# Optimization experiments

Measured on AMD Instinct MI355X. Metric: run time of the kernel, lower is better.

Reference implementation:

```python
import jax, jax.numpy as jnp
import numpy as np

POOL = (7, 7)


def crop_and_resize(image, boxes, box_idx, crop_size):
    """Faithful jnp port of tf.image.crop_and_resize (bilinear, extrapolation_value=0).

    image: [B, H, W, C]; boxes: [N, 4] normalized (y1, x1, y2, x2); box_idx: [N] int.
    Returns [N, ph, pw, C].
    """
    H, W = image.shape[1], image.shape[2]
    ph, pw = crop_size
    y1, x1, y2, x2 = boxes[:, 0], boxes[:, 1], boxes[:, 2], boxes[:, 3]
    iy = jnp.arange(ph, dtype=image.dtype)
    ix = jnp.arange(pw, dtype=image.dtype)
    # sample coords in source-pixel space, TF convention for crop_size > 1
    ys = y1[:, None] * (H - 1) + iy[None, :] * ((y2 - y1)[:, None] * (H - 1) / (ph - 1))  # [N, ph]
    xs = x1[:, None] * (W - 1) + ix[None, :] * ((x2 - x1)[:, None] * (W - 1) / (pw - 1))  # [N, pw]
    vy = (ys >= 0) & (ys <= H - 1)
    vx = (xs >= 0) & (xs <= W - 1)
    y0 = jnp.floor(ys)
    x0 = jnp.floor(xs)
    wy = (ys - y0)[:, :, None, None]   # [N, ph, 1, 1]
    wx = (xs - x0)[:, None, :, None]   # [N, 1, pw, 1]
    y0i = jnp.clip(y0, 0, H - 1).astype(jnp.int32)
    y1i = jnp.clip(y0 + 1, 0, H - 1).astype(jnp.int32)  # when ys is integral, wy==0 so clamp is harmless
    x0i = jnp.clip(x0, 0, W - 1).astype(jnp.int32)
    x1i = jnp.clip(x0 + 1, 0, W - 1).astype(jnp.int32)
    b = box_idx[:, None, None]

    def g(yi, xi):
        return image[b, yi[:, :, None], xi[:, None, :], :]  # [N, ph, pw, C]

    top = g(y0i, x0i) * (1 - wx) + g(y0i, x1i) * wx
    bot = g(y1i, x0i) * (1 - wx) + g(y1i, x1i) * wx
    out = top * (1 - wy) + bot * wy
    valid = (vy[:, :, None] & vx[:, None, :])[..., None]
    return jnp.where(valid, out, jnp.zeros((), image.dtype))


def setup_inputs() -> dict:
    key = jax.random.key(0)
    kb, kp, k3, k4, k5 = jax.random.split(key, 5)
    B, N, C = 2, 1000, 256
    # valid normalized boxes: per-axis sorted uniforms -> y1 <= y2, x1 <= x2
    raw = jax.random.uniform(kb, (B, N, 2, 2), dtype=jnp.float32)  # [..., (y|x), (lo,hi)]
    raw = jnp.sort(raw, axis=-1)
    boxes = jnp.stack([raw[..., 0, 0], raw[..., 1, 0], raw[..., 0, 1], raw[..., 1, 1]], axis=-1)
    return {
        "boxes": boxes,
        "positive_indices": jax.random.randint(kp, (B, N), 0, 2, dtype=jnp.int32),
        "p3": jax.random.normal(k3, (B, 128, 128, C), dtype=jnp.float32),
        "p4": jax.random.normal(k4, (B, 64, 64, C), dtype=jnp.float32),
        "p5": jax.random.normal(k5, (B, 32, 32, C), dtype=jnp.float32),
        "config": 0,
    }


def reference(boxes, positive_indices, p3, p4, p5, config):
    B, N = boxes.shape[0], boxes.shape[1]
    ph, pw = POOL
    h = boxes[..., 2] - boxes[..., 0]
    w = boxes[..., 3] - boxes[..., 1]
    # roi_level = clip(ceil(5 + log2(h*w)), 3, 5); clip in float first (log2(0) -> -inf)
    lvl = jnp.ceil(5.0 + jnp.log(h * w) / jnp.log(2.0))
    roi_level = jnp.clip(lvl, 3.0, 5.0).astype(jnp.int32)  # [B, N]
    boxes_flat = jax.lax.stop_gradient(boxes.reshape(B * N, 4))  # boxes get no grad in original
    lvl_flat = roi_level.reshape(B * N)
    box_idx = jnp.repeat(jnp.arange(B, dtype=jnp.int32), N)
    C = p3.shape[-1]
    pooled = jnp.zeros((B * N, ph, pw, C), dtype=p3.dtype)
    for level, feat in zip((3, 4, 5), (p3, p4, p5)):
        crop = crop_and_resize(feat, boxes_flat, box_idx, POOL)
        mask = (lvl_flat == level)[:, None, None, None]
        pooled = jnp.where(mask, crop, pooled)
    return pooled.reshape(B, N, ph, pw, C)
```

## Files before the change

### kernel.cpp

```cpp
#include <hip/hip_runtime.h>
#include <math.h>


#define N_PER_B 1000
#define NBOX    2000
#define CCH     256
#define PH      7
#define PW      7

typedef float f4 __attribute__((ext_vector_type(4)));

__global__ __launch_bounds__(448, 2) void pyramid_roi_align_kernel(
    const float* __restrict__ boxes,
    const float* __restrict__ p3,
    const float* __restrict__ p4,
    const float* __restrict__ p5,
    float* __restrict__ out)
{
    const int box  = blockIdx.x;
    const int iy   = threadIdx.x >> 6;
    const int lane = threadIdx.x & 63;
    const int c    = lane * 4;

    const float y1 = boxes[box * 4 + 0];
    const float x1 = boxes[box * 4 + 1];
    const float y2 = boxes[box * 4 + 2];
    const float x2 = boxes[box * 4 + 3];
    const float h  = y2 - y1;
    const float w  = x2 - x1;

    const float lvl  = ceilf(5.0f + logf(h * w) / 0.69314718055994530942f);
    const float lvlc = fminf(fmaxf(lvl, 3.0f), 5.0f);
    const int level  = (int)lvlc;

    const float* feat;
    int H;
    if (level <= 3)      { feat = p3; H = 128; }
    else if (level == 4) { feat = p4; H = 64;  }
    else                 { feat = p5; H = 32;  }
    const int W = H;

    const int b = (box >= N_PER_B) ? 1 : 0;
    feat += (size_t)b * H * W * CCH;

    const float Hm1 = (float)(H - 1);
    const float Wm1 = (float)(W - 1);

    const float ys = y1 * Hm1 + (float)iy * (h * Hm1 / 6.0f);
    const bool  vy = (ys >= 0.0f) && (ys <= Hm1);

    const float y0f = floorf(ys);
    const float wy  = ys - y0f;
    const float omwy = 1.0f - wy;

    const int y0i = (int)fminf(fmaxf(y0f,        0.0f), Hm1);
    const int y1i = (int)fminf(fmaxf(y0f + 1.0f, 0.0f), Hm1);

    const float* row0 = feat + (size_t)y0i * W * CCH + c;
    const float* row1 = feat + (size_t)y1i * W * CCH + c;

    const float xstep = w * Wm1 / 6.0f;

    int   x0i[PW], x1i[PW];
    float wxv[PW];
    bool  vx[PW];
#pragma unroll
    for (int ix = 0; ix < PW; ++ix) {
        const float xs = x1 * Wm1 + (float)ix * xstep;
        vx[ix] = (xs >= 0.0f) && (xs <= Wm1);
        const float x0f = floorf(xs);
        wxv[ix] = xs - x0f;
        x0i[ix] = (int)fminf(fmaxf(x0f,        0.0f), Wm1);
        x1i[ix] = (int)fminf(fmaxf(x0f + 1.0f, 0.0f), Wm1);
    }

    f4 v00[PW], v01[PW], v10[PW], v11[PW];
#pragma unroll
    for (int ix = 0; ix < PW; ++ix) {
        v00[ix] = *(const f4*)(row0 + (size_t)x0i[ix] * CCH);
        v01[ix] = *(const f4*)(row0 + (size_t)x1i[ix] * CCH);
        v10[ix] = *(const f4*)(row1 + (size_t)x0i[ix] * CCH);
        v11[ix] = *(const f4*)(row1 + (size_t)x1i[ix] * CCH);
    }

    float* dst_base = out + ((size_t)box * (PH * PW) + (size_t)iy * PW) * CCH + c;

#pragma unroll
    for (int ix = 0; ix < PW; ++ix) {
        const float wx   = wxv[ix];
        const float omwx = 1.0f - wx;

        f4 res = (v00[ix] * omwx + v01[ix] * wx) * omwy
               + (v10[ix] * omwx + v11[ix] * wx) * wy;

        if (!(vy && vx[ix])) res = (f4)(0.0f);

        __builtin_nontemporal_store(res, (f4*)(dst_base + (size_t)ix * CCH));
    }
}

extern "C" void kernel_launch(void* const* d_in, const int* in_sizes, int n_in,
                              void* d_out, int out_size, void* d_ws, size_t ws_size,
                              hipStream_t stream) {
    const float* boxes = (const float*)d_in[0];
    const float* p3 = (const float*)d_in[2];
    const float* p4 = (const float*)d_in[3];
    const float* p5 = (const float*)d_in[4];
    float* out = (float*)d_out;

    hipLaunchKernelGGL(pyramid_roi_align_kernel, dim3(NBOX), dim3(448), 0, stream,
                       boxes, p3, p4, p5, out);
}
```

Measured before the change: 171.2 us.

## Bucket boxes by level, batch and y-band and swizzle blocks across XCDs

Adds a single-block pre-pass that bucket-sorts boxes by pyramid level, batch index and vertical center band into a permutation held in workspace. The main kernel reads boxes through this permutation, and a block-id swizzle gives each XCD a contiguous chunk of sorted boxes, so boxes that sample the same feature rows share an L2. The output store also changes from nontemporal to a normal store. In exchange it adds an extra kernel launch and a serial prefix sum, and it depends on workspace being available.

Result: slower. 177.2 us (+3.5%).

```diff
diff --git a/kernel.cpp b/kernel.cpp
--- a/kernel.cpp
+++ b/kernel.cpp
@@ -8,16 +8,75 @@
 #define PH      7
 #define PW      7
 
+#define NXCD    8
+#define CHUNK   (NBOX / NXCD)
+
+#define NBUCKET 96
+
 typedef float f4 __attribute__((ext_vector_type(4)));
+
+__device__ __forceinline__ int box_level(float h, float w) {
+    const float lvl  = ceilf(5.0f + logf(h * w) / 0.69314718055994530942f);
+    const float lvlc = fminf(fmaxf(lvl, 3.0f), 5.0f);
+    return (int)lvlc;
+}
+
+__global__ __launch_bounds__(1024) void sort_boxes_kernel(
+    const float* __restrict__ boxes, int* __restrict__ perm)
+{
+    __shared__ int cnt[NBUCKET];
+    __shared__ int base[NBUCKET];
+    const int t = threadIdx.x;
+    if (t < NBUCKET) cnt[t] = 0;
+    __syncthreads();
+
+    int mykey[2];
+#pragma unroll
+    for (int i = 0; i < 2; ++i) {
+        const int box = t + i * 1024;
+        int key = -1;
+        if (box < NBOX) {
+            const float y1 = boxes[box * 4 + 0];
+            const float x1 = boxes[box * 4 + 1];
+            const float y2 = boxes[box * 4 + 2];
+            const float x2 = boxes[box * 4 + 3];
+            const int level = box_level(y2 - y1, x2 - x1);
+            const int b     = (box >= N_PER_B) ? 1 : 0;
+            const float cy  = 0.5f * (y1 + y2);
+            const int yband = (int)fminf(fmaxf(cy * 16.0f, 0.0f), 15.0f);
+            key = ((level - 3) * 2 + b) * 16 + yband;
+            atomicAdd(&cnt[key], 1);
+        }
+        mykey[i] = key;
+    }
+    __syncthreads();
+    if (t == 0) {
+        int acc = 0;
+        for (int k = 0; k < NBUCKET; ++k) { base[k] = acc; acc += cnt[k]; }
+    }
+    __syncthreads();
+#pragma unroll
+    for (int i = 0; i < 2; ++i) {
+        const int box = t + i * 1024;
+        if (box < NBOX) {
+            const int pos = atomicAdd(&base[mykey[i]], 1);
+            perm[pos] = box;
+        }
+    }
+}
 
 __global__ __launch_bounds__(448, 2) void pyramid_roi_align_kernel(
     const float* __restrict__ boxes,
     const float* __restrict__ p3,
     const float* __restrict__ p4,
     const float* __restrict__ p5,
+    const int*   __restrict__ perm,
     float* __restrict__ out)
 {
-    const int box  = blockIdx.x;
+    const int bid = blockIdx.x;
+    const int swz = (bid & (NXCD - 1)) * CHUNK + (bid >> 3);
+    const int box = perm ? perm[swz] : swz;
+
     const int iy   = threadIdx.x >> 6;
     const int lane = threadIdx.x & 63;
     const int c    = lane * 4;
@@ -29,9 +88,7 @@
     const float h  = y2 - y1;
     const float w  = x2 - x1;
 
-    const float lvl  = ceilf(5.0f + logf(h * w) / 0.69314718055994530942f);
-    const float lvlc = fminf(fmaxf(lvl, 3.0f), 5.0f);
-    const int level  = (int)lvlc;
+    const int level = box_level(h, w);
 
     const float* feat;
     int H;
@@ -95,7 +152,7 @@
 
         if (!(vy && vx[ix])) res = (f4)(0.0f);
 
-        __builtin_nontemporal_store(res, (f4*)(dst_base + (size_t)ix * CCH));
+        *(f4*)(dst_base + (size_t)ix * CCH) = res;
     }
 }
 
@@ -108,6 +165,13 @@
     const float* p5 = (const float*)d_in[4];
     float* out = (float*)d_out;
 
+    int* perm = nullptr;
+    if (d_ws != nullptr && ws_size >= (size_t)NBOX * sizeof(int)) {
+        perm = (int*)d_ws;
+        hipLaunchKernelGGL(sort_boxes_kernel, dim3(1), dim3(1024), 0, stream,
+                           boxes, perm);
+    }
+
     hipLaunchKernelGGL(pyramid_roi_align_kernel, dim3(NBOX), dim3(448), 0, stream,
-                       boxes, p3, p4, p5, out);
+                       boxes, p3, p4, p5, perm, out);
 }
```
